# Kernel optimization log

Measured on AMD Instinct MI355X. Metric: run time of the kernel, lower is better.

## Reference

```python
import jax, jax.numpy as jnp
import numpy as np

VEC_DIM = 128   # D (also the per-head dim in this module)
HEADS = 8
PATCH = 4
WIN = 7
N_BATCH = 4
H_IMG = 448
W_IMG = 448


def _relative_index():
    # Swin-style relative position index, computed statically (matches torch code
    # which uses torch.meshgrid with default 'ij' indexing).
    coords = np.stack(np.meshgrid(np.arange(WIN), np.arange(WIN), indexing='ij'))  # [2,W,W]
    flat = coords.reshape(2, -1)                      # [2, W*W]
    rel = flat[:, :, None] - flat[:, None, :]         # [2, p, p]
    rel = rel.transpose(1, 2, 0).astype(np.int64)     # [p, p, 2]
    rel[:, :, 0] += WIN - 1
    rel[:, :, 1] += WIN - 1
    rel[:, :, 1] *= 2 * WIN - 1
    return rel.sum(-1)                                # [p, p], values in [0, (2W-1)^2)

REL_IDX = jnp.asarray(_relative_index())


def setup_inputs() -> dict:
    key = jax.random.key(0)
    ks = jax.random.split(key, 8)
    P = (H_IMG // PATCH) * (W_IMG // PATCH)  # 12544
    D, H = VEC_DIM, HEADS
    s = 0.02
    return {
        'x': jax.random.normal(ks[0], (N_BATCH, D, P), jnp.float32),
        'Wq': jax.random.normal(ks[1], (H * D, D), jnp.float32) * s,
        'bq': jnp.zeros((H * D,), jnp.float32),
        'Wk': jax.random.normal(ks[2], (H * D, D), jnp.float32) * s,
        'bk': jnp.zeros((H * D,), jnp.float32),
        'Wv': jax.random.normal(ks[3], (H * D, D), jnp.float32) * s,
        'bv': jnp.zeros((H * D,), jnp.float32),
        'Wo': jax.random.normal(ks[4], (D, H * D), jnp.float32) * s,
        'bo': jnp.zeros((D,), jnp.float32),
        'pos_code': jax.random.normal(ks[5], ((2 * WIN - 1) ** 2, H), jnp.float32) * s,
        'h': H_IMG,
        'w': W_IMG,
    }


def reference(x, Wq, bq, Wk, bk, Wv, bv, Wo, bo, pos_code, h, w):
    N, D, P = x.shape
    H = HEADS
    ch, cw = h // PATCH, w // PATCH
    nh, nw = ch // WIN, cw // WIN            # windows per axis
    p = WIN * WIN                            # tokens per window

    def emb(W, b):
        # pointwise Conv1d: [N,D,P] -> [N,H*D,P] -> [N,H,D,P]
        return (jnp.einsum('od,ndp->nop', W, x) + b[None, :, None]).reshape(N, H, D, P)

    def partition(e):
        # [N,H,D,P] -> [N,H,win_num,D,p]
        e = e.reshape(N, H, D, nh, WIN, nw, WIN)
        return e.transpose(0, 1, 3, 5, 2, 4, 6).reshape(N, H, nh * nw, D, p)

    q = partition(emb(Wq, bq))
    k = partition(emb(Wk, bk))
    v = partition(emb(Wv, bv))

    # attn[n,h,w,i,j] = sum_d k[n,h,w,d,i] * q[n,h,w,d,j], scaled
    attn = jnp.einsum('nhwdi,nhwdj->nhwij', k, q) / (D ** 0.5)
    bias = pos_code[REL_IDX].transpose(2, 0, 1)          # [H, p, p]
    attn = attn + bias[None, :, None, :, :]
    weights = jax.nn.softmax(attn, axis=3)               # softmax over key index i

    # out[n,h,w,d,j] = sum_i v[n,h,w,d,i] * weights[n,h,w,i,j]
    out = jnp.einsum('nhwdi,nhwij->nhwdj', v, weights)

    # window merge: [N,H,win_num,D,p] -> [N,H*D,P]
    out = out.reshape(N, H, nh, nw, D, WIN, WIN)
    out = out.transpose(0, 1, 4, 2, 5, 3, 6).reshape(N, H * D, P)

    return jnp.einsum('od,ndp->nop', Wo, out) + bo[None, :, None]
```

## Files before the change

### kernel.cpp

```cpp
#include <hip/hip_runtime.h>
#include <hip/hip_bf16.h>

typedef unsigned short u16;
typedef unsigned int u32;
typedef __attribute__((ext_vector_type(8))) short bf16x8;
typedef __attribute__((ext_vector_type(4))) float f32x4;
typedef __attribute__((ext_vector_type(2))) unsigned int u32x2;

#define NBATCH 4
#define DDIM   128
#define NHEAD  8
#define PTOT   12544
#define CWID   112
#define NTOK   49
#define PSTR   68
#define SCALE  0.08838834764831845f

#define BUFSZ   14464
#undef BUFSZ
#define BUFSZ   16384
#define OFF_US  8192
#define OFF_PL  32768
#define OFF_PCF 36100
#define OFF_MF  38804
#define OFF_CS  40852
#define LDS_TOT 41876

#undef OFF_MF
#undef OFF_CS
#undef LDS_TOT
#define OFF_CS  38804
#define LDS_TOT 39828

__device__ __forceinline__ float bf2f(u16 u) {
    union { u32 i; float f; } x; x.i = ((u32)u) << 16; return x.f;
}
__device__ __forceinline__ u16 f2bf(float f) {
    union { float f; u32 u; } v; v.f = f;
    return (u16)((v.u + 0x7fffu + ((v.u >> 16) & 1u)) >> 16);
}
__device__ __forceinline__ u32 pk2(float a, float b) {
    union { __hip_bfloat162 h; u32 u; } c;
    float2 t; t.x = a; t.y = b;
    c.h = __float22bfloat162_rn(t);
    return c.u;
}
__device__ __forceinline__ int swz128(int row, int col) {
    return row * 128 + ((((col >> 3) ^ (row & 15)) & 15) << 3) + (col & 7);
}

#define WS_WC   131072
#define WS_F32  262144

__global__ void __launch_bounds__(256) prep(
    const float* __restrict__ Wq, const float* __restrict__ Wk,
    const float* __restrict__ Wv, const float* __restrict__ Wo,
    const float* __restrict__ bq, const float* __restrict__ bk,
    const float* __restrict__ bv, u16* __restrict__ ws)
{
    __shared__ u16 lm[32768];
    const int tid = threadIdx.x;
    const int b = blockIdx.x;
    const bool isG = (b >= 8);
    const int h = b & 7;
    float* fb = (float*)(ws + WS_F32);

    if (!isG) {
        for (int idx = tid; idx < 16384; idx += 256) {
            const int dd = idx >> 7, dh = idx & 127;
            lm[swz128(dd, dh)] = f2bf(Wo[dd * 1024 + h * 128 + dh]);
        }
        for (int idx = tid; idx < 16384; idx += 256) {
            const int dh = idx >> 7, d = idx & 127;
            lm[16384 + swz128(d, dh)] = f2bf(Wv[(h * 128 + dh) * 128 + d]);
        }
        if (tid < 128) {
            float s = 0.f;
            for (int dh = 0; dh < 128; ++dh)
                s += Wo[tid * 1024 + h * 128 + dh] * bv[h * 128 + dh];
            fb[h * 128 + tid] = s;
        }
    } else {
        for (int idx = tid; idx < 16384; idx += 256) {
            const int dh = idx >> 7, d = idx & 127;
            lm[swz128(d, dh)] = f2bf(Wk[(h * 128 + dh) * 128 + d]);
        }
        for (int idx = tid; idx < 16384; idx += 256) {
            const int dh = idx >> 7, dp = idx & 127;
            lm[16384 + swz128(dp, dh)] = f2bf(Wq[(h * 128 + dh) * 128 + dp]);
        }
        if (tid < 128) {
            float r = 0.f, m = 0.f;
            for (int dh = 0; dh < 128; ++dh) {
                r += bk[h * 128 + dh] * Wq[(h * 128 + dh) * 128 + tid];
                m += Wk[(h * 128 + dh) * 128 + tid] * bq[h * 128 + dh];
            }
            fb[1024 + h * 128 + tid] = r * SCALE;
            fb[2048 + h * 128 + tid] = m * SCALE;
        }
        if (tid == 0) {
            float s = 0.f;
            for (int dh = 0; dh < 128; ++dh) s += bk[h * 128 + dh] * bq[h * 128 + dh];
            fb[3072 + h] = s * SCALE;
        }
    }
    __syncthreads();

    const int w = tid >> 6, lane = tid & 63, quad = lane >> 4, lid = lane & 15;
    const f32x4 z4 = {0.f, 0.f, 0.f, 0.f};
    u16* dst = ws + (isG ? 0 : WS_WC) + h * 16384;
    const float gs = isG ? SCALE : 1.0f;
    #pragma unroll
    for (int mtl = 0; mtl < 2; ++mtl) {
        const int mt = 2 * w + mtl;
        bf16x8 A[4];
        #pragma unroll
        for (int kt = 0; kt < 4; ++kt)
            A[kt] = *(const bf16x8*)(lm + swz128(mt * 16 + lid, kt * 32 + quad * 8));
        #pragma unroll
        for (int nt = 0; nt < 8; ++nt) {
            f32x4 acc = z4;
            #pragma unroll
            for (int kt = 0; kt < 4; ++kt) {
                bf16x8 B = *(const bf16x8*)(lm + 16384 + swz128(nt * 16 + lid, kt * 32 + quad * 8));
                acc = __builtin_amdgcn_mfma_f32_16x16x32_bf16(A[kt], B, acc, 0, 0, 0);
            }
            #pragma unroll
            for (int r = 0; r < 4; ++r) {
                const int row = mt * 16 + quad * 4 + r, col = nt * 16 + lid;
                if (isG) dst[col * 128 + row] = f2bf(acc[r] * gs);
                else     dst[row * 128 + col] = f2bf(acc[r]);
            }
        }
    }
}

__global__ void __launch_bounds__(256, 2)
winattn(const float* __restrict__ xg, const u16* __restrict__ ws,
        const float* __restrict__ bo, const float* __restrict__ posf,
        float* __restrict__ out)
{
    __shared__ __align__(16) u16 sm[LDS_TOT];
    u16* xw  = sm;
    u16* pl  = sm + OFF_PL;
    float* pcf = (float*)(sm + OFF_PCF);
    float* cs  = (float*)(sm + OFF_CS);

    const int tid  = threadIdx.x;
    const int w    = tid >> 6;
    const int lane = tid & 63;
    const int quad = lane >> 4;
    const int lid  = lane & 15;
    const int bx   = blockIdx.x;
    const int n    = bx >> 8;
    const int win  = bx & 255;
    const int pbase = (win >> 4) * 7 * CWID + (win & 15) * 7;

    const bf16x8 zf = {0,0,0,0,0,0,0,0};
    const f32x4  z4 = {0.f,0.f,0.f,0.f};

    const u16* Gt  = ws;
    const u16* Wcw = ws + WS_WC;
    const float* fb  = (const float*)(ws + WS_F32);
    const float* bcv = fb;
    const float* rP  = fb + 1024;
    const float* MP  = fb + 2048;
    const float* sP  = fb + 3072;

    for (int i = tid; i < 169 * NHEAD; i += 256) pcf[i] = posf[i];
    const float* xn = xg + n * DDIM * PTOT;
    for (int idx = tid; idx < DDIM * NTOK; idx += 256) {
        int d = idx / NTOK;
        int t = idx - d * NTOK;
        int a = t / 7, b = t - a * 7;
        xw[swz128(t, d)] = f2bf(xn[d * PTOT + pbase + a * CWID + b]);
    }
    __syncthreads();

    bf16x8 xfrag[4][4];
    #pragma unroll
    for (int mt = 0; mt < 4; ++mt)
        #pragma unroll
        for (int kt = 0; kt < 4; ++kt)
            xfrag[mt][kt] = (mt * 16 + lid < NTOK)
                ? *(const bf16x8*)(xw + swz128(mt * 16 + lid, kt * 32 + quad * 8)) : zf;
    const int j = 16 * w + lid;
    bf16x8 xq[4];
    #pragma unroll
    for (int kt = 0; kt < 4; ++kt)
        xq[kt] = (j < NTOK)
            ? *(const bf16x8*)(xw + swz128(j, kt * 32 + quad * 8)) : zf;

    for (int hh = w; hh < NHEAD; hh += 4) {
        const float sh = sP[hh];
        #pragma unroll
        for (int mt = 0; mt < 4; ++mt) {
            float c = 0.f;
            #pragma unroll
            for (int kt = 0; kt < 4; ++kt)
                #pragma unroll
                for (int jj = 0; jj < 8; ++jj)
                    c += bf2f((u16)xfrag[mt][kt][jj]) * MP[hh * 128 + kt * 32 + quad * 8 + jj];
            c += __shfl_xor(c, 16);
            c += __shfl_xor(c, 32);
            if (quad == 0) cs[hh * 64 + mt * 16 + lid] = c + sh;
        }
    }
    __syncthreads();

    f32x4 outacc[8];
    #pragma unroll
    for (int nt = 0; nt < 8; ++nt) outacc[nt] = z4;

    const int jc = j < NTOK ? j : NTOK - 1;

    for (int h = 0; h < NHEAD; ++h) {
        u16* tsb = sm + (h & 1) * BUFSZ;
        u16* usb = tsb + OFF_US;

        #pragma unroll
        for (int mtl = 0; mtl < 2; ++mtl) {
            const int mt = 2 * w + mtl;
            bf16x8 A[4];
            #pragma unroll
            for (int kt = 0; kt < 4; ++kt)
                A[kt] = *(const bf16x8*)(Gt + h * 16384 + (mt * 16 + lid) * 128 + kt * 32 + quad * 8);
            const f32x4 rb = *(const f32x4*)(rP + h * 128 + mt * 16 + quad * 4);
            const int dpb = mt * 16 + quad * 4;
            #pragma unroll
            for (int nt = 0; nt < 4; ++nt) {
                f32x4 acc = z4;
                #pragma unroll
                for (int kt = 0; kt < 4; ++kt)
                    acc = __builtin_amdgcn_mfma_f32_16x16x32_bf16(A[kt], xfrag[nt][kt], acc, 0, 0, 0);
                const int i = nt * 16 + lid;
                u32x2 pkv;
                pkv.x = pk2(acc[0] + rb[0], acc[1] + rb[1]);
                pkv.y = pk2(acc[2] + rb[2], acc[3] + rb[3]);
                *(u32x2*)(tsb + i * 128 + ((((dpb >> 3) ^ (i & 15)) & 15) << 3) + (dpb & 7)) = pkv;
            }
        }
        #pragma unroll
        for (int ntl = 0; ntl < 2; ++ntl) {
            const int nt = 2 * w + ntl;
            bf16x8 B[4];
            #pragma unroll
            for (int kt = 0; kt < 4; ++kt)
                B[kt] = *(const bf16x8*)(Wcw + h * 16384 + (nt * 16 + lid) * 128 + kt * 32 + quad * 8);
            const int dd = nt * 16 + lid;
            const float bb = bcv[h * 128 + dd];
            #pragma unroll
            for (int mt = 0; mt < 4; ++mt) {
                f32x4 acc = z4;
                #pragma unroll
                for (int kt = 0; kt < 4; ++kt)
                    acc = __builtin_amdgcn_mfma_f32_16x16x32_bf16(xfrag[mt][kt], B[kt], acc, 0, 0, 0);
                const int ib = mt * 16 + quad * 4;
                u32x2 pkv;
                pkv.x = pk2(acc[0] + bb, acc[1] + bb);
                pkv.y = pk2(acc[2] + bb, acc[3] + bb);
                *(u32x2*)(usb + dd * 64 + ((((ib >> 3) ^ (dd & 7)) & 7) << 3) + (ib & 7)) = pkv;
            }
        }
        __syncthreads();

        f32x4 S[4];
        #pragma unroll
        for (int mt = 0; mt < 4; ++mt) {
            S[mt] = z4;
            #pragma unroll
            for (int kt = 0; kt < 4; ++kt) {
                bf16x8 A = *(const bf16x8*)(tsb + (mt * 16 + lid) * 128 + ((((kt * 4 + quad) ^ lid) & 15) << 3));
                S[mt] = __builtin_amdgcn_mfma_f32_16x16x32_bf16(A, xq[kt], S[mt], 0, 0, 0);
            }
        }
        const int aj = jc / 7, bj = jc - aj * 7;
        float sv[4][4];
        float mx = -3.0e38f;
        #pragma unroll
        for (int mt = 0; mt < 4; ++mt)
            #pragma unroll
            for (int r = 0; r < 4; ++r) {
                const int ii = mt * 16 + quad * 4 + r;
                float vvv;
                if (ii < NTOK) {
                    const int ai = ii / 7, bi = ii - ai * 7;
                    const int rel = (ai - aj + 6) + 13 * (bi - bj + 6);
                    vvv = S[mt][r] + cs[h * 64 + ii] + pcf[rel * NHEAD + h];
                } else {
                    vvv = -3.0e38f;
                }
                sv[mt][r] = vvv;
                mx = fmaxf(mx, vvv);
            }
        mx = fmaxf(mx, __shfl_xor(mx, 16));
        mx = fmaxf(mx, __shfl_xor(mx, 32));
        float ssum = 0.f;
        #pragma unroll
        for (int mt = 0; mt < 4; ++mt)
            #pragma unroll
            for (int r = 0; r < 4; ++r) {
                const float e = __expf(sv[mt][r] - mx);
                sv[mt][r] = e;
                ssum += e;
            }
        ssum += __shfl_xor(ssum, 16);
        ssum += __shfl_xor(ssum, 32);
        const float inv = 1.0f / ssum;
        if (j < NTOK) {
            #pragma unroll
            for (int mt = 0; mt < 4; ++mt) {
                u32x2 pkv;
                pkv.x = pk2(sv[mt][0] * inv, sv[mt][1] * inv);
                pkv.y = pk2(sv[mt][2] * inv, sv[mt][3] * inv);
                *(u32x2*)(pl + j * PSTR + mt * 16 + quad * 4) = pkv;
            }
        }
        __threadfence_block();

        #pragma unroll
        for (int kt = 0; kt < 2; ++kt) {
            union { bf16x8 v; u32 u[4]; } Af;
            #pragma unroll
            for (int q2 = 0; q2 < 4; ++q2)
                Af.u[q2] = *(const u32*)(pl + jc * PSTR + kt * 32 + quad * 8 + 2 * q2);
            #pragma unroll
            for (int nt = 0; nt < 8; ++nt) {
                const int dd = nt * 16 + lid;
                bf16x8 Bu = *(const bf16x8*)(usb + dd * 64 + ((((kt * 4 + quad) ^ (dd & 7)) & 7) << 3));
                outacc[nt] = __builtin_amdgcn_mfma_f32_16x16x32_bf16(Af.v, Bu, outacc[nt], 0, 0, 0);
            }
        }
    }

    float* outp = out + n * DDIM * PTOT;
    #pragma unroll
    for (int nt = 0; nt < 8; ++nt) {
        const int dd = nt * 16 + lid;
        const float bov = bo[dd];
        #pragma unroll
        for (int r = 0; r < 4; ++r) {
            const int jj = 16 * w + quad * 4 + r;
            if (jj < NTOK) {
                const int a = jj / 7, b = jj - a * 7;
                outp[dd * PTOT + pbase + a * CWID + b] = outacc[nt][r] + bov;
            }
        }
    }
}

extern "C" void kernel_launch(void* const* d_in, const int* in_sizes, int n_in,
                              void* d_out, int out_size, void* d_ws, size_t ws_size,
                              hipStream_t stream) {
    (void)in_sizes; (void)n_in; (void)ws_size; (void)out_size;
    prep<<<16, 256, 0, stream>>>((const float*)d_in[1], (const float*)d_in[3],
                                 (const float*)d_in[5], (const float*)d_in[7],
                                 (const float*)d_in[2], (const float*)d_in[4],
                                 (const float*)d_in[6], (u16*)d_ws);
    winattn<<<NBATCH * 256, 256, 0, stream>>>(
        (const float*)d_in[0], (const u16*)d_ws,
        (const float*)d_in[8], (const float*)d_in[9], (float*)d_out);
}
```

Baseline: 236.0 us.

## Single-buffer head LDS, drop softmax max pass, widen prep to 1024 threads

Result: slower. 314.7 us (+33.4%).

```diff
diff --git a/kernel.cpp b/kernel.cpp
--- a/kernel.cpp
+++ b/kernel.cpp
@@ -16,21 +16,12 @@
 #define PSTR   68
 #define SCALE  0.08838834764831845f
 
-#define BUFSZ   14464
-#undef BUFSZ
-#define BUFSZ   16384
+#define OFF_TS  0
 #define OFF_US  8192
-#define OFF_PL  32768
-#define OFF_PCF 36100
-#define OFF_MF  38804
-#define OFF_CS  40852
-#define LDS_TOT 41876
-
-#undef OFF_MF
-#undef OFF_CS
-#undef LDS_TOT
-#define OFF_CS  38804
-#define LDS_TOT 39828
+#define OFF_PL  16384
+#define OFF_PCF 19716
+#define OFF_CS  22420
+#define LDS_TOT 23444
 
 __device__ __forceinline__ float bf2f(u16 u) {
     union { u32 i; float f; } x; x.i = ((u32)u) << 16; return x.f;
@@ -52,7 +43,7 @@
 #define WS_WC   131072
 #define WS_F32  262144
 
-__global__ void __launch_bounds__(256) prep(
+__global__ void __launch_bounds__(1024) prep(
     const float* __restrict__ Wq, const float* __restrict__ Wk,
     const float* __restrict__ Wv, const float* __restrict__ Wo,
     const float* __restrict__ bq, const float* __restrict__ bk,
@@ -66,11 +57,11 @@
     float* fb = (float*)(ws + WS_F32);
 
     if (!isG) {
-        for (int idx = tid; idx < 16384; idx += 256) {
+        for (int idx = tid; idx < 16384; idx += 1024) {
             const int dd = idx >> 7, dh = idx & 127;
             lm[swz128(dd, dh)] = f2bf(Wo[dd * 1024 + h * 128 + dh]);
         }
-        for (int idx = tid; idx < 16384; idx += 256) {
+        for (int idx = tid; idx < 16384; idx += 1024) {
             const int dh = idx >> 7, d = idx & 127;
             lm[16384 + swz128(d, dh)] = f2bf(Wv[(h * 128 + dh) * 128 + d]);
         }
@@ -81,11 +72,11 @@
             fb[h * 128 + tid] = s;
         }
     } else {
-        for (int idx = tid; idx < 16384; idx += 256) {
+        for (int idx = tid; idx < 16384; idx += 1024) {
             const int dh = idx >> 7, d = idx & 127;
             lm[swz128(d, dh)] = f2bf(Wk[(h * 128 + dh) * 128 + d]);
         }
-        for (int idx = tid; idx < 16384; idx += 256) {
+        for (int idx = tid; idx < 16384; idx += 1024) {
             const int dh = idx >> 7, dp = idx & 127;
             lm[16384 + swz128(dp, dh)] = f2bf(Wq[(h * 128 + dh) * 128 + dp]);
         }
@@ -106,42 +97,42 @@
     }
     __syncthreads();
 
-    const int w = tid >> 6, lane = tid & 63, quad = lane >> 4, lid = lane & 15;
+    const int w16 = tid >> 6, lane = tid & 63, quad = lane >> 4, lid = lane & 15;
+    const int mt = w16 >> 1, nt0 = (w16 & 1) * 4;
     const f32x4 z4 = {0.f, 0.f, 0.f, 0.f};
     u16* dst = ws + (isG ? 0 : WS_WC) + h * 16384;
     const float gs = isG ? SCALE : 1.0f;
-    #pragma unroll
-    for (int mtl = 0; mtl < 2; ++mtl) {
-        const int mt = 2 * w + mtl;
-        bf16x8 A[4];
-        #pragma unroll
-        for (int kt = 0; kt < 4; ++kt)
-            A[kt] = *(const bf16x8*)(lm + swz128(mt * 16 + lid, kt * 32 + quad * 8));
-        #pragma unroll
-        for (int nt = 0; nt < 8; ++nt) {
-            f32x4 acc = z4;
-            #pragma unroll
-            for (int kt = 0; kt < 4; ++kt) {
-                bf16x8 B = *(const bf16x8*)(lm + 16384 + swz128(nt * 16 + lid, kt * 32 + quad * 8));
-                acc = __builtin_amdgcn_mfma_f32_16x16x32_bf16(A[kt], B, acc, 0, 0, 0);
-            }
-            #pragma unroll
-            for (int r = 0; r < 4; ++r) {
-                const int row = mt * 16 + quad * 4 + r, col = nt * 16 + lid;
-                if (isG) dst[col * 128 + row] = f2bf(acc[r] * gs);
-                else     dst[row * 128 + col] = f2bf(acc[r]);
-            }
-        }
-    }
-}
-
-__global__ void __launch_bounds__(256, 2)
+    bf16x8 A[4];
+    #pragma unroll
+    for (int kt = 0; kt < 4; ++kt)
+        A[kt] = *(const bf16x8*)(lm + swz128(mt * 16 + lid, kt * 32 + quad * 8));
+    #pragma unroll
+    for (int ntl = 0; ntl < 4; ++ntl) {
+        const int nt = nt0 + ntl;
+        f32x4 acc = z4;
+        #pragma unroll
+        for (int kt = 0; kt < 4; ++kt) {
+            bf16x8 B = *(const bf16x8*)(lm + 16384 + swz128(nt * 16 + lid, kt * 32 + quad * 8));
+            acc = __builtin_amdgcn_mfma_f32_16x16x32_bf16(A[kt], B, acc, 0, 0, 0);
+        }
+        #pragma unroll
+        for (int r = 0; r < 4; ++r) {
+            const int row = mt * 16 + quad * 4 + r, col = nt * 16 + lid;
+            if (isG) dst[col * 128 + row] = f2bf(acc[r] * gs);
+            else     dst[row * 128 + col] = f2bf(acc[r]);
+        }
+    }
+}
+
+__global__ void __launch_bounds__(256, 3)
 winattn(const float* __restrict__ xg, const u16* __restrict__ ws,
         const float* __restrict__ bo, const float* __restrict__ posf,
         float* __restrict__ out)
 {
     __shared__ __align__(16) u16 sm[LDS_TOT];
     u16* xw  = sm;
+    u16* tsb = sm + OFF_TS;
+    u16* usb = sm + OFF_US;
     u16* pl  = sm + OFF_PL;
     float* pcf = (float*)(sm + OFF_PCF);
     float* cs  = (float*)(sm + OFF_CS);
@@ -215,9 +206,6 @@
     const int jc = j < NTOK ? j : NTOK - 1;
 
     for (int h = 0; h < NHEAD; ++h) {
-        u16* tsb = sm + (h & 1) * BUFSZ;
-        u16* usb = tsb + OFF_US;
-
         #pragma unroll
         for (int mtl = 0; mtl < 2; ++mtl) {
             const int mt = 2 * w + mtl;
@@ -276,31 +264,18 @@
         }
         const int aj = jc / 7, bj = jc - aj * 7;
         float sv[4][4];
-        float mx = -3.0e38f;
+        float ssum = 0.f;
         #pragma unroll
         for (int mt = 0; mt < 4; ++mt)
             #pragma unroll
             for (int r = 0; r < 4; ++r) {
                 const int ii = mt * 16 + quad * 4 + r;
-                float vvv;
+                float e = 0.f;
                 if (ii < NTOK) {
                     const int ai = ii / 7, bi = ii - ai * 7;
                     const int rel = (ai - aj + 6) + 13 * (bi - bj + 6);
-                    vvv = S[mt][r] + cs[h * 64 + ii] + pcf[rel * NHEAD + h];
-                } else {
-                    vvv = -3.0e38f;
+                    e = __expf(S[mt][r] + cs[h * 64 + ii] + pcf[rel * NHEAD + h]);
                 }
-                sv[mt][r] = vvv;
-                mx = fmaxf(mx, vvv);
-            }
-        mx = fmaxf(mx, __shfl_xor(mx, 16));
-        mx = fmaxf(mx, __shfl_xor(mx, 32));
-        float ssum = 0.f;
-        #pragma unroll
-        for (int mt = 0; mt < 4; ++mt)
-            #pragma unroll
-            for (int r = 0; r < 4; ++r) {
-                const float e = __expf(sv[mt][r] - mx);
                 sv[mt][r] = e;
                 ssum += e;
             }
@@ -331,6 +306,7 @@
                 outacc[nt] = __builtin_amdgcn_mfma_f32_16x16x32_bf16(Af.v, Bu, outacc[nt], 0, 0, 0);
             }
         }
+        __syncthreads();
     }
 
     float* outp = out + n * DDIM * PTOT;
@@ -353,10 +329,10 @@
                               void* d_out, int out_size, void* d_ws, size_t ws_size,
                               hipStream_t stream) {
     (void)in_sizes; (void)n_in; (void)ws_size; (void)out_size;
-    prep<<<16, 256, 0, stream>>>((const float*)d_in[1], (const float*)d_in[3],
-                                 (const float*)d_in[5], (const float*)d_in[7],
-                                 (const float*)d_in[2], (const float*)d_in[4],
-                                 (const float*)d_in[6], (u16*)d_ws);
+    prep<<<16, 1024, 0, stream>>>((const float*)d_in[1], (const float*)d_in[3],
+                                  (const float*)d_in[5], (const float*)d_in[7],
+                                  (const float*)d_in[2], (const float*)d_in[4],
+                                  (const float*)d_in[6], (u16*)d_ws);
     winattn<<<NBATCH * 256, 256, 0, stream>>>(
         (const float*)d_in[0], (const u16*)d_ws,
         (const float*)d_in[8], (const float*)d_in[9], (float*)d_out);
```
